# Kernel optimization log

Hardware: AMD Instinct MI355X
Metric: run time of the kernel (lower is better)

## Reference

```python
import jax, jax.numpy as jnp
import numpy as np

B, RES, C = 4, 128, 256
HW = RES * RES
H_FFT, W_FFT = RES, RES // 2 + 1
NUM_BANDS, GATE_HIDDEN = 6, 128
LN_EPS = 1e-5
FFT_NORM = 'ortho'
INIT_RANGE = 0.02


def _band_info(h_fft, w_fft, nb):
    # static radial band partition of the rFFT2 plane (matches RadialBandGate.__init__)
    yy = np.arange(h_fft, dtype=np.float32)[:, None] / max(h_fft - 1, 1)
    xx = np.arange(w_fft, dtype=np.float32)[None, :] / max(w_fft - 1, 1)
    r = np.sqrt(yy ** 2 + xx ** 2)
    r = r / (r.max() + 1e-8)
    bid = np.minimum(np.floor(r * nb), nb - 1).astype(np.int32).reshape(-1)  # (F,)
    onehot = np.zeros((bid.size, nb), dtype=np.float32)
    onehot[np.arange(bid.size), bid] = 1.0
    counts = np.maximum(onehot.sum(0), 1.0)
    return jnp.asarray(bid), jnp.asarray(onehot), jnp.asarray(counts)

BAND_ID, BAND_ONEHOT, BAND_COUNTS = _band_info(H_FFT, W_FFT, NUM_BANDS)


def setup_inputs() -> dict:
    key = jax.random.key(0)
    ks = jax.random.split(key, 16)
    return {
        'x': jax.random.normal(ks[0], (B, HW, C), jnp.float32),
        'time': jax.random.uniform(ks[1], (B,), jnp.float32),
        'w_real': jax.random.normal(ks[2], (C, C), jnp.float32) * INIT_RANGE,
        'w_imag': jax.random.normal(ks[3], (C, C), jnp.float32) * INIT_RANGE,
        'conv_w': jax.random.normal(ks[4], (C, 1, 3, 3), jnp.float32) * 0.1,  # depthwise
        'lin_w': jax.random.normal(ks[5], (C, C), jnp.float32) * 0.02,
        'lin_b': jnp.zeros((C,), jnp.float32),
        'mlp_w1': jax.random.normal(ks[6], (GATE_HIDDEN, NUM_BANDS), jnp.float32) * 0.3,
        'mlp_b1': jnp.zeros((GATE_HIDDEN,), jnp.float32),
        'mlp_w2': jax.random.normal(ks[7], (NUM_BANDS, GATE_HIDDEN), jnp.float32) * 0.1,
        'mlp_b2': jnp.zeros((NUM_BANDS,), jnp.float32),
        'norm_ww': jax.random.normal(ks[8], (C, 1), jnp.float32) * 0.02,  # ConditionalLayerNorm.weight Linear(1,dim)
        'norm_wb': jnp.ones((C,), jnp.float32),
        'norm_bw': jax.random.normal(ks[9], (C, 1), jnp.float32) * 0.02,
        'norm_bb': jnp.zeros((C,), jnp.float32),
        'kx': jnp.asarray(0.25, jnp.float32),
        'ky': jnp.asarray(0.25, jnp.float32),
    }


def _band_gate(feat, mlp_w1, mlp_b1, mlp_w2, mlp_b2):
    # feat: (B, C, F) real. scatter-add per band via one-hot matmul, mean, MLP, gather back.
    sums = jnp.einsum('bcf,fn->bcn', feat, BAND_ONEHOT)           # (B,C,NB)
    means = sums / (BAND_COUNTS + 1e-6)
    h = jax.nn.relu(jnp.einsum('bcn,hn->bch', means, mlp_w1) + mlp_b1)
    alpha_band = jax.nn.sigmoid(jnp.einsum('bch,nh->bcn', h, mlp_w2) + mlp_b2)
    return alpha_band[:, :, BAND_ID]                               # (B,C,F)


def reference(x, time, w_real, w_imag, conv_w, lin_w, lin_b,
              mlp_w1, mlp_b1, mlp_w2, mlp_b2,
              norm_ww, norm_wb, norm_bw, norm_bb, kx, ky):
    h = w = RES
    x2 = jnp.transpose(x.reshape(B, h, w, C), (0, 3, 1, 2))        # (B,C,h,w)
    Xf = jnp.fft.rfft2(x2, norm=FFT_NORM)                          # (B,C,h_fft,w_fft) complex

    # low-frequency rectangular mask (int(sigmoid(k)*dim) == floor for positive values)
    kx_i = jnp.floor(jax.nn.sigmoid(kx) * H_FFT)
    ky_i = jnp.floor(jax.nn.sigmoid(ky) * W_FFT)
    mask = ((jnp.arange(H_FFT)[:, None] < kx_i) & (jnp.arange(W_FFT)[None, :] < ky_i))
    Xf_low = Xf * mask[None, None].astype(Xf.real.dtype)

    F = H_FFT * W_FFT
    Xf_low_flat = Xf_low.reshape(B, C, F)
    W = w_real + 1j * w_imag                                       # (C,C) complex
    Xf_low_mapped = jnp.einsum('cd,bdf->bcf', W, Xf_low_flat).reshape(B, C, H_FFT, W_FFT)

    Xf_high = Xf - Xf_low
    feat_pred = jnp.abs(jnp.abs(Xf_high).reshape(B, C, F) - jnp.abs(Xf_low).reshape(B, C, F))
    alpha = _band_gate(feat_pred, mlp_w1, mlp_b1, mlp_w2, mlp_b2).reshape(B, C, H_FFT, W_FFT)

    Xf_fused = alpha * Xf_low_mapped + (1.0 - alpha) * Xf_high
    x_spec = jnp.fft.irfft2(Xf_fused, s=(h, w), norm=FFT_NORM)     # (B,C,h,w) real

    # depthwise 3x3 conv, padding=1, no bias
    xl = jax.lax.conv_general_dilated(x2, conv_w, window_strides=(1, 1), padding='SAME',
                                      feature_group_count=C,
                                      dimension_numbers=('NCHW', 'OIHW', 'NCHW'))
    # pointwise linear over channel dim
    xc = jnp.transpose((x @ lin_w.T + lin_b).reshape(B, h, w, C), (0, 3, 1, 2))

    y = jnp.transpose(x_spec + xl + xc, (0, 2, 3, 1)).reshape(B, HW, C)

    # ConditionalLayerNorm
    mean = y.mean(axis=-1, keepdims=True)
    var = (y ** 2).mean(axis=-1, keepdims=True) - mean ** 2
    yn = (y - mean) / jnp.sqrt(var + LN_EPS)
    t = time.reshape(-1, 1)                                        # (B,1)
    weight = (t @ norm_ww.T + norm_wb)[:, None, :]                 # (B,1,C)
    bias = (t @ norm_bw.T + norm_bb)[:, None, :]
    return weight * yn + bias
```

## Files before the change

kernel.cpp:

```cpp
#include <hip/hip_runtime.h>
#include <math.h>

#define B_ 4
#define C_ 256
#define RES_ 128
#define HW_ 16384
#define WF_ 65
#define F_ 8320
#define FP_ 2880

typedef __attribute__((ext_vector_type(8))) short bf16x8;
typedef __attribute__((ext_vector_type(16))) float f32x16;

__device__ __forceinline__ int brev6(int j){ return (int)(__brev((unsigned)j) >> 26); }

__device__ __forceinline__ short f2bf(float f){
  unsigned u = __float_as_uint(f);
  unsigned r = (u + 0x7FFFu + ((u>>16)&1u)) >> 16;
  return (short)r;
}

__device__ __forceinline__ bf16x8 lds_frag(const short* p){
  union { bf16x8 v; int2 d[2]; } u;
  u.d[0] = *(const int2*)p;
  u.d[1] = *(const int2*)(p+4);
  return u.v;
}
__device__ __forceinline__ void lds_store8(short* p, bf16x8 v){
  union { bf16x8 v; int2 d[2]; } u; u.v = v;
  *(int2*)p = u.d[0]; *(int2*)(p+4) = u.d[1];
}

__device__ __forceinline__ int band_of(int row, int col){
  float yy = __fdiv_rn((float)row, 127.0f);
  float xx = __fdiv_rn((float)col, 64.0f);
  float rr = __fsqrt_rn(__fadd_rn(__fmul_rn(yy,yy), __fmul_rn(xx,xx)));
  float rm = __fadd_rn(__fsqrt_rn(2.0f), 1e-8f);
  float rn = __fdiv_rn(rr, rm);
  int b = (int)floorf(__fmul_rn(rn, 6.0f));
  return b > 5 ? 5 : b;
}

__device__ __forceinline__ float sigmoidf_(float v){ return 1.0f/(1.0f+expf(-v)); }

template<int SGN>
__device__ __forceinline__ float2 wave_fft64(float2 v, const float2* stw, int lane){
  #pragma unroll
  for (int s=0; s<6; s++){
    int H = 32 >> s;
    float ox = __shfl_xor(v.x, H);
    float oy = __shfl_xor(v.y, H);
    bool hi = (lane & H) != 0;
    float2 w = stw[s];
    float ws = (SGN < 0) ? -w.y : w.y;
    float sx = v.x + ox, sy = v.y + oy;
    float dx = ox - v.x, dy = oy - v.y;
    float rx = dx*w.x - dy*ws;
    float ry = dx*ws + dy*w.x;
    v.x = hi ? rx : sx;
    v.y = hi ? ry : sy;
  }
  return v;
}

__device__ __forceinline__ void make_stage_tw(float2* stw, int lane){
  #pragma unroll
  for (int s=0; s<6; s++){
    int H = 32 >> s;
    int t = (lane & (H-1)) << s;
    float sn, cs;
    sincosf(6.283185307179586f*(float)t/64.0f, &sn, &cs);
    stw[s] = make_float2(cs, sn);
  }
}

__device__ __forceinline__ void redist2(float2 a0, float2 a1, int lane, float2& u0, float2& u1){
  int s0 = lane >> 1, s1 = s0 + 32;
  bool odd = (lane & 1) != 0;
  float t0x = __shfl(a0.x, s0), t0y = __shfl(a0.y, s0);
  float t1x = __shfl(a1.x, s0), t1y = __shfl(a1.y, s0);
  u0 = odd ? make_float2(t1x, t1y) : make_float2(t0x, t0y);
  float q0x = __shfl(a0.x, s1), q0y = __shfl(a0.y, s1);
  float q1x = __shfl(a1.x, s1), q1y = __shfl(a1.y, s1);
  u1 = odd ? make_float2(q1x, q1y) : make_float2(q0x, q0y);
}

__global__ __launch_bounds__(256) void k_transpose(const float* __restrict__ x, float* __restrict__ x2){
  __shared__ float tile[64][68];
  int b = blockIdx.z;
  int hw0 = blockIdx.x*64, c0 = blockIdx.y*64;
  int tid = threadIdx.x;
  #pragma unroll
  for (int q=0;q<4;q++){
    int p = tid + q*256;
    int hw = p >> 4, c4 = (p & 15) << 2;
    float4 v = *(const float4*)&x[((size_t)b*HW_ + hw0 + hw)*C_ + c0 + c4];
    *(float4*)&tile[hw][c4] = v;
  }
  __syncthreads();
  #pragma unroll
  for (int q=0;q<4;q++){
    int p = tid + q*256;
    int c = p >> 4, h4 = (p & 15) << 2;
    float4 v = make_float4(tile[h4][c], tile[h4+1][c], tile[h4+2][c], tile[h4+3][c]);
    *(float4*)&x2[((size_t)b*C_ + c0 + c)*HW_ + hw0 + h4] = v;
  }
}

__global__ __launch_bounds__(256) void k_counts(float* __restrict__ counts, unsigned char* __restrict__ bid_t){
  int tid = threadIdx.x;
  float acc[6] = {0,0,0,0,0,0};
  for (int p = tid; p < F_; p += 256){
    int kx = p >> 7, ky = p & 127;
    int bnd = band_of(ky, kx);
    bid_t[p] = (unsigned char)bnd;
    #pragma unroll
    for (int n=0;n<6;n++) acc[n] += (bnd==n) ? 1.0f : 0.0f;
  }
  __shared__ float red[6][256];
  #pragma unroll
  for (int n=0;n<6;n++) red[n][tid] = acc[n];
  __syncthreads();
  for (int s=128; s>0; s>>=1){
    if (tid < s){
      #pragma unroll
      for (int n=0;n<6;n++) red[n][tid] += red[n][tid+s];
    }
    __syncthreads();
  }
  if (tid < 6) counts[tid] = fmaxf(red[tid][0], 1.0f);
}

__global__ __launch_bounds__(256) void k_wbf16(const float* __restrict__ wre, const float* __restrict__ wim,
                                               const float* __restrict__ lw,
                                               short* __restrict__ Wre, short* __restrict__ Wim,
                                               short* __restrict__ WL){
  int c = blockIdx.x, tid = threadIdx.x, plane = blockIdx.y;
  int idx = c*C_ + tid;
  if (plane == 0)      Wre[idx] = f2bf(wre[idx]);
  else if (plane == 1) Wim[idx] = f2bf(wim[idx]);
  else                 WL[idx]  = f2bf(lw[idx]);
}

__global__ __launch_bounds__(256) void k_fwd_rows(const float* __restrict__ x2, float2* __restrict__ X1t){
  __shared__ float2 tile[65*33];
  int tid = threadIdx.x;
  int lane = tid & 63, wv = tid >> 6;
  float2 stw[6];
  make_stage_tw(stw, lane);
  float sn128, cs128;
  sincosf(6.283185307179586f*(float)lane/128.0f, &sn128, &cs128);
  int slice = blockIdx.x >> 2;
  int r0 = (blockIdx.x & 3) * 32;
  const float* img = x2 + (size_t)slice*HW_ + (size_t)r0*128;
  #pragma unroll
  for (int i=0; i<8; i++){
    int rr = wv*8 + i;
    float2 y = *(const float2*)(img + rr*128 + lane*2);
    float2 v = wave_fft64<-1>(y, stw, lane);
    int rbk = brev6(lane);
    float2 Yk; Yk.x = __shfl(v.x, rbk); Yk.y = __shfl(v.y, rbk);
    int rbm = brev6((64 - lane) & 63);
    float2 Ym; Ym.x = __shfl(v.x, rbm); Ym.y = __shfl(v.y, rbm);
    float sx = Yk.x + Ym.x, sy = Yk.y - Ym.y;
    float dx = Yk.x - Ym.x, dy = Yk.y + Ym.y;
    tile[lane*33 + rr] = make_float2(0.5f*(sx - sn128*dx + cs128*dy),
                                     0.5f*(sy - cs128*dx - sn128*dy));
    if (lane == 0)
      tile[64*33 + rr] = make_float2(Yk.x - Yk.y, 0.0f);
  }
  __syncthreads();
  float2* dst = X1t + (size_t)slice*F_ + r0;
  for (int p = tid; p < 65*16; p += 256){
    int kx = p >> 4, r2 = (p & 15) << 1;
    float2 a = tile[kx*33 + r2], b = tile[kx*33 + r2 + 1];
    *(float4*)(dst + (size_t)kx*128 + r2) = make_float4(a.x, a.y, b.x, b.y);
  }
}

__global__ __launch_bounds__(256) void k_fwd_cols_gate(const float2* __restrict__ X1t, float2* __restrict__ Xft,
                                                       const float* __restrict__ counts, const unsigned char* __restrict__ bid_t,
                                                       const float* __restrict__ w1, const float* __restrict__ b1,
                                                       const float* __restrict__ w2, const float* __restrict__ b2,
                                                       float* __restrict__ alpha){
  __shared__ float red[6][4];
  __shared__ float means[6], h[128];
  int tid = threadIdx.x;
  int lane = tid & 63, wv = tid >> 6;
  float2 stw[6];
  make_stage_tw(stw, lane);
  float sn128, cs128;
  sincosf(6.283185307179586f*(float)lane/128.0f, &sn128, &cs128);
  int slice = blockIdx.x;
  const float2* xin = X1t + (size_t)slice*F_;
  float2* xout = Xft + (size_t)slice*F_;
  float acc[6] = {0,0,0,0,0,0};
  for (int kx = wv; kx < 65; kx += 4){
    float4 rv = *(const float4*)(xin + (size_t)kx*128 + (lane<<1));
    float2 a0 = make_float2(rv.x, rv.y), a1 = make_float2(rv.z, rv.w);
    float2 u0, u1;
    redist2(a0, a1, lane, u0, u1);
    float2 s = make_float2(u0.x+u1.x, u0.y+u1.y);
    float ddx = u0.x-u1.x, ddy = u0.y-u1.y;
    float2 dw = make_float2(ddx*cs128 + ddy*sn128, ddy*cs128 - ddx*sn128);
    float2 v0 = wave_fft64<-1>(s, stw, lane);
    float2 v1 = wave_fft64<-1>(dw, stw, lane);
    int rb = brev6(lane);
    float ex = __shfl(v0.x, rb), ey = __shfl(v0.y, rb);
    float ox = __shfl(v1.x, rb), oy = __shfl(v1.y, rb);
    ex *= 0.0078125f; ey *= 0.0078125f;
    ox *= 0.0078125f; oy *= 0.0078125f;
    float4 wvout = make_float4(ex, ey, ox, oy);
    *(float4*)(xout + (size_t)kx*128 + (lane<<1)) = wvout;
    float me = __fsqrt_rn(ex*ex + ey*ey);
    float mo = __fsqrt_rn(ox*ox + oy*oy);
    int be = (int)bid_t[kx*128 + (lane<<1)];
    int bo = (int)bid_t[kx*128 + (lane<<1) + 1];
    #pragma unroll
    for (int n=0;n<6;n++) acc[n] += ((be==n) ? me : 0.0f) + ((bo==n) ? mo : 0.0f);
  }
  #pragma unroll
  for (int n=0;n<6;n++){
    float v = acc[n];
    #pragma unroll
    for (int off=32; off>0; off>>=1) v += __shfl_xor(v, off);
    if (lane == 0) red[n][wv] = v;
  }
  __syncthreads();
  if (tid < 6) means[tid] = (red[tid][0]+red[tid][1]+red[tid][2]+red[tid][3]) / (counts[tid] + 1e-6f);
  __syncthreads();
  if (tid < 128){
    float hv = b1[tid];
    #pragma unroll
    for (int n=0;n<6;n++) hv += means[n]*w1[tid*6+n];
    h[tid] = fmaxf(hv, 0.0f);
  }
  __syncthreads();
  if (tid < 6){
    float o = b2[tid];
    for (int j=0;j<128;j++) o += h[j]*w2[tid*128+j];
    alpha[slice*6 + tid] = sigmoidf_(o);
  }
}

__global__ __launch_bounds__(256) void k_xt(const float2* __restrict__ Xft,
                                            short* __restrict__ XtRe, short* __restrict__ XtIm){
  __shared__ short sre[72*130];
  __shared__ short sim[72*130];
  int tid = threadIdx.x;
  int kx = blockIdx.x, d0 = blockIdx.y*128, b = blockIdx.z;
  const float2* xb = Xft + ((size_t)(b*C_ + d0))*F_ + (size_t)kx*128;
  for (int p = tid; p < 72*128; p += 256){
    int d = p / 72, ky = p - d*72;
    float2 v = xb[(size_t)d*F_ + ky];
    sre[ky*130 + d] = f2bf(v.x);
    sim[ky*130 + d] = f2bf(v.y);
  }
  __syncthreads();
  short* dre = XtRe + ((size_t)b*FP_ + (size_t)kx*72)*C_ + d0;
  short* dim_ = XtIm + ((size_t)b*FP_ + (size_t)kx*72)*C_ + d0;
  for (int p = tid; p < 72*128; p += 256){
    int ky = p >> 7, d = p & 127;
    dre[(size_t)ky*C_ + d] = sre[ky*130 + d];
    dim_[(size_t)ky*C_ + d] = sim[ky*130 + d];
  }
}

__global__ __launch_bounds__(256) void k_mix_mfma(const short* __restrict__ Wre, const short* __restrict__ Wim,
                                                  const short* __restrict__ XtRe, const short* __restrict__ XtIm,
                                                  const float* __restrict__ kxp, const float* __restrict__ kyp,
                                                  float2* __restrict__ mappedP){
  __shared__ short Are[64][36], Aim[64][36], Bre[64][36], Bim[64][36];
  int tid = threadIdx.x;
  int fp0 = blockIdx.x*64, c0 = blockIdx.y*64, b = blockIdx.z;
  int lane = tid & 63, w = tid >> 6;
  int mt = (w >> 1)*32, nt = (w & 1)*32;
  f32x16 accre = {0.f,0.f,0.f,0.f,0.f,0.f,0.f,0.f,0.f,0.f,0.f,0.f,0.f,0.f,0.f,0.f};
  f32x16 accim = {0.f,0.f,0.f,0.f,0.f,0.f,0.f,0.f,0.f,0.f,0.f,0.f,0.f,0.f,0.f,0.f};
  const short* xrb = XtRe + ((size_t)b*FP_ + fp0)*C_;
  const short* xib = XtIm + ((size_t)b*FP_ + fp0)*C_;
  int row4 = tid >> 2, part = tid & 3;
  for (int kc=0; kc<8; kc++){
    int d0 = kc*32;
    __syncthreads();
    lds_store8(&Are[row4][part*8], *(const bf16x8*)&Wre[(c0+row4)*C_ + d0 + part*8]);
    lds_store8(&Aim[row4][part*8], *(const bf16x8*)&Wim[(c0+row4)*C_ + d0 + part*8]);
    lds_store8(&Bre[row4][part*8], *(const bf16x8*)&xrb[(size_t)row4*C_ + d0 + part*8]);
    lds_store8(&Bim[row4][part*8], *(const bf16x8*)&xib[(size_t)row4*C_ + d0 + part*8]);
    __syncthreads();
    #pragma unroll
    for (int ks=0; ks<2; ks++){
      int koff = ks*16 + (lane>>5)*8;
      bf16x8 are = lds_frag(&Are[mt + (lane&31)][koff]);
      bf16x8 aim = lds_frag(&Aim[mt + (lane&31)][koff]);
      bf16x8 bre = lds_frag(&Bre[nt + (lane&31)][koff]);
      bf16x8 bim = lds_frag(&Bim[nt + (lane&31)][koff]);
      bf16x8 naim;
      { union { bf16x8 v; unsigned u[4]; } t1, t2; t1.v = aim;
        #pragma unroll
        for (int j=0;j<4;j++) t2.u[j] = t1.u[j] ^ 0x80008000u;
        naim = t2.v; }
      accre = __builtin_amdgcn_mfma_f32_32x32x16_bf16(are,  bre, accre, 0,0,0);
      accre = __builtin_amdgcn_mfma_f32_32x32x16_bf16(naim, bim, accre, 0,0,0);
      accim = __builtin_amdgcn_mfma_f32_32x32x16_bf16(are,  bim, accim, 0,0,0);
      accim = __builtin_amdgcn_mfma_f32_32x32x16_bf16(aim,  bre, accim, 0,0,0);
    }
  }
  float rowlim = floorf(sigmoidf_(kxp[0])*128.0f);
  float collim = floorf(sigmoidf_(kyp[0])*65.0f);
  int n = fp0 + nt + (lane & 31);
  int ky = n % 72, kx = n / 72;
  bool live = ((float)ky < rowlim) && ((float)kx < collim);
  #pragma unroll
  for (int reg=0; reg<16; reg++){
    int r = (reg & 3) + 8*(reg >> 2) + 4*(lane >> 5);
    int c = c0 + mt + r;
    if (live)
      mappedP[((size_t)(b*C_ + c))*FP_ + n] = make_float2(accre[reg], accim[reg]);
  }
}

__global__ __launch_bounds__(256) void k_pw_mfma(const float* __restrict__ x, const short* __restrict__ WL,
                                                  const float* __restrict__ lb, float* __restrict__ xcs){
  __shared__ short As[64][36], Bs[64][36];
  int tid = threadIdx.x;
  int hw0 = blockIdx.x*64, c0 = blockIdx.y*64, b = blockIdx.z;
  int lane = tid & 63, w = tid >> 6;
  int mt = (w >> 1)*32, nt = (w & 1)*32;
  f32x16 acc = {0.f,0.f,0.f,0.f,0.f,0.f,0.f,0.f,0.f,0.f,0.f,0.f,0.f,0.f,0.f,0.f};
  const float* xb = x + ((size_t)b*HW_ + hw0)*C_;
  int row4 = tid >> 2, part = tid & 3;
  for (int kc=0; kc<8; kc++){
    int d0 = kc*32;
    __syncthreads();
    lds_store8(&As[row4][part*8], *(const bf16x8*)&WL[(c0+row4)*C_ + d0 + part*8]);
    {
      const float* src = &xb[(size_t)row4*C_ + d0 + part*8];
      float4 va = *(const float4*)src;
      float4 vb = *(const float4*)(src+4);
      bf16x8 bv;
      bv[0]=f2bf(va.x); bv[1]=f2bf(va.y); bv[2]=f2bf(va.z); bv[3]=f2bf(va.w);
      bv[4]=f2bf(vb.x); bv[5]=f2bf(vb.y); bv[6]=f2bf(vb.z); bv[7]=f2bf(vb.w);
      lds_store8(&Bs[row4][part*8], bv);
    }
    __syncthreads();
    #pragma unroll
    for (int ks=0; ks<2; ks++){
      int koff = ks*16 + (lane>>5)*8;
      bf16x8 a  = lds_frag(&As[mt + (lane&31)][koff]);
      bf16x8 bb = lds_frag(&Bs[nt + (lane&31)][koff]);
      acc = __builtin_amdgcn_mfma_f32_32x32x16_bf16(a, bb, acc, 0,0,0);
    }
  }
  int n = hw0 + nt + (lane & 31);
  #pragma unroll
  for (int reg=0; reg<16; reg++){
    int r = (reg & 3) + 8*(reg >> 2) + 4*(lane >> 5);
    int c = c0 + mt + r;
    xcs[((size_t)(b*C_ + c))*HW_ + n] = acc[reg] + lb[c];
  }
}

__global__ __launch_bounds__(256) void k_inv_cols(float2* __restrict__ XftY, const float2* __restrict__ mappedP,
                                                  const float* __restrict__ alpha, const unsigned char* __restrict__ bid_t,
                                                  const float* __restrict__ kxp, const float* __restrict__ kyp){
  __shared__ float al[6];
  int tid = threadIdx.x;
  int lane = tid & 63, wv = tid >> 6;
  int slice = blockIdx.x;
  float2 stw[6];
  make_stage_tw(stw, lane);
  float sn128, cs128;
  sincosf(6.283185307179586f*(float)lane/128.0f, &sn128, &cs128);
  if (tid < 6) al[tid] = alpha[slice*6 + tid];
  float rowlim = floorf(sigmoidf_(kxp[0])*128.0f);
  float collim = floorf(sigmoidf_(kyp[0])*65.0f);
  __syncthreads();
  float2* xfb = XftY + (size_t)slice*F_;
  const float2* mpb = mappedP + (size_t)slice*FP_;
  for (int kx = wv; kx < 65; kx += 4){
    float4 rv = *(const float4*)(xfb + (size_t)kx*128 + (lane<<1));
    int ky0 = lane << 1;
    float a_e = al[(int)bid_t[kx*128 + ky0]];
    float a_o = al[(int)bid_t[kx*128 + ky0 + 1]];
    bool cok  = ((float)kx < collim);
    bool in_e = cok && ((float)ky0 < rowlim);
    bool in_o = cok && ((float)(ky0+1) < rowlim);
    float2 ve, vo;
    if (in_e){
      float4 mv = *(const float4*)(mpb + (size_t)kx*72 + ky0);
      ve = make_float2(mv.x*a_e, mv.y*a_e);
      vo = in_o ? make_float2(mv.z*a_o, mv.w*a_o)
                : make_float2(rv.z*(1.0f-a_o), rv.w*(1.0f-a_o));
    } else {
      ve = make_float2(rv.x*(1.0f-a_e), rv.y*(1.0f-a_e));
      vo = make_float2(rv.z*(1.0f-a_o), rv.w*(1.0f-a_o));
    }
    float2 u0, u1;
    redist2(ve, vo, lane, u0, u1);
    float2 s = make_float2(u0.x+u1.x, u0.y+u1.y);
    float ddx = u0.x-u1.x, ddy = u0.y-u1.y;
    float2 dw = make_float2(ddx*cs128 - ddy*sn128, ddx*sn128 + ddy*cs128);
    float2 v0 = wave_fft64<1>(s, stw, lane);
    float2 v1 = wave_fft64<1>(dw, stw, lane);
    int rb = brev6(lane);
    float4 outv;
    outv.x = __shfl(v0.x, rb); outv.y = __shfl(v0.y, rb);
    outv.z = __shfl(v1.x, rb); outv.w = __shfl(v1.y, rb);
    *(float4*)(xfb + (size_t)kx*128 + (lane<<1)) = outv;
  }
}

__global__ __launch_bounds__(256,8) void k_inv_rows(const float2* __restrict__ Y1t, const float* __restrict__ xcs,
                                                    const float* __restrict__ x2, const float* __restrict__ cw,
                                                    float* __restrict__ sbuf){
  __shared__ float2 ytile[65*33];
  int tid = threadIdx.x;
  int lane = tid & 63, wv = tid >> 6;
  float2 stw[6];
  make_stage_tw(stw, lane);
  float sn128, cs128;
  sincosf(6.283185307179586f*(float)lane/128.0f, &sn128, &cs128);
  int slice = blockIdx.x >> 2;
  int ch = slice & 255;
  int r0 = (blockIdx.x & 3) * 32;
  const float* img = x2 + (size_t)slice*HW_;
  int base = r0 + wv*8;
  float2 rows[10];
  #pragma unroll
  for (int i=0;i<10;i++){
    int gr = base - 1 + i;
    rows[i] = ((unsigned)gr < 128u) ? *(const float2*)(img + (size_t)gr*128 + (lane<<1))
                                    : make_float2(0.0f, 0.0f);
  }
  const float2* ysrc = Y1t + (size_t)slice*F_ + r0;
  for (int p = tid; p < 65*16; p += 256){
    int kx = p >> 4, r2 = (p & 15) << 1;
    float4 v = *(const float4*)(ysrc + (size_t)kx*128 + r2);
    ytile[kx*33 + r2]     = make_float2(v.x, v.y);
    ytile[kx*33 + r2 + 1] = make_float2(v.z, v.w);
  }
  float w9[9];
  #pragma unroll
  for (int k=0;k<9;k++) w9[k] = cw[ch*9+k];
  __syncthreads();
  size_t gbase = (size_t)slice*HW_ + (size_t)r0*128;
  #pragma unroll
  for (int i=0;i<8;i++){
    int row = wv*8 + i;
    float2 a = ytile[lane*33 + row];
    float2 b = ytile[(64-lane)*33 + row];
    if (lane == 0){ a.y = 0.0f; b.y = 0.0f; }
    float sx = a.x + b.x, sy = a.y - b.y;
    float dx = a.x - b.x, dy = a.y + b.y;
    float2 yk = make_float2(0.5f*(sx - sn128*dx - cs128*dy),
                            0.5f*(sy + cs128*dx - sn128*dy));
    float2 v = wave_fft64<1>(yk, stw, lane);
    int rbk = brev6(lane);
    float2 z; z.x = __shfl(v.x, rbk); z.y = __shfl(v.y, rbk);
    int xx = lane << 1;
    float c0 = 0.0f, c1 = 0.0f;
    #pragma unroll
    for (int dy2=0; dy2<3; dy2++){
      float2 cv = rows[i + dy2];
      float l = __shfl_up(cv.y, 1);
      if (lane == 0) l = 0.0f;
      float r = __shfl_down(cv.x, 1);
      if (lane == 63) r = 0.0f;
      c0 += l*w9[dy2*3+0] + cv.x*w9[dy2*3+1] + cv.y*w9[dy2*3+2];
      c1 += cv.x*w9[dy2*3+0] + cv.y*w9[dy2*3+1] + r*w9[dy2*3+2];
    }
    size_t g = gbase + (size_t)(row*128 + xx);
    float2 xc = *(const float2*)&xcs[g];
    float2 o;
    o.x = z.x*0.015625f + xc.x + c0;
    o.y = z.y*0.015625f + xc.y + c1;
    *(float2*)&sbuf[g] = o;
  }
}

__global__ __launch_bounds__(256) void k_norm(const float* __restrict__ sbuf, const float* __restrict__ timev,
                                              const float* __restrict__ nww, const float* __restrict__ nwb,
                                              const float* __restrict__ nbw, const float* __restrict__ nbb,
                                              float* __restrict__ out){
  __shared__ float tile[64][65];
  __shared__ float p1[64][5], p2[64][5];
  __shared__ float mv[64], rv[64], wv_[256], bv_[256];
  int b = blockIdx.y, hw0 = blockIdx.x*64;
  int tid = threadIdx.x;
  {
    float t = timev[b];
    wv_[tid] = t*nww[tid] + nwb[tid];
    bv_[tid] = t*nbw[tid] + nbb[tid];
  }
  int hwl = tid & 63, cg = tid >> 6;
  const float* p = sbuf + (size_t)b*C_*HW_ + hw0 + hwl;
  float s1 = 0.0f, s2 = 0.0f;
  for (int c = cg*64; c < cg*64 + 64; c++){
    float v = p[(size_t)c*HW_];
    s1 += v; s2 += v*v;
  }
  p1[hwl][cg] = s1; p2[hwl][cg] = s2;
  __syncthreads();
  if (tid < 64){
    float t1 = p1[tid][0] + p1[tid][1] + p1[tid][2] + p1[tid][3];
    float t2 = p2[tid][0] + p2[tid][1] + p2[tid][2] + p2[tid][3];
    float mean = t1 * (1.0f/256.0f);
    float var  = t2 * (1.0f/256.0f) - mean*mean;
    mv[tid] = mean;
    rv[tid] = 1.0f / sqrtf(var + 1e-5f);
  }
  __syncthreads();
  for (int cg2=0; cg2<4; cg2++){
    int c0 = cg2*64;
    #pragma unroll
    for (int q=0;q<16;q++){
      int pp = tid + q*256;
      int cl = pp >> 6, hl = pp & 63;
      tile[cl][hl] = sbuf[((size_t)(b*C_ + c0 + cl))*HW_ + hw0 + hl];
    }
    __syncthreads();
    #pragma unroll
    for (int q=0;q<16;q++){
      int pp = tid + q*256;
      int hl = pp >> 6, cl = pp & 63;
      float v = tile[cl][hl];
      out[((size_t)(b*HW_ + hw0 + hl))*C_ + c0 + cl] = wv_[c0+cl]*((v - mv[hl])*rv[hl]) + bv_[c0+cl];
    }
    __syncthreads();
  }
}

extern "C" void kernel_launch(void* const* d_in, const int* in_sizes, int n_in,
                              void* d_out, int out_size, void* d_ws, size_t ws_size,
                              hipStream_t stream){
  const float* x      = (const float*)d_in[0];
  const float* timev  = (const float*)d_in[1];
  const float* w_real = (const float*)d_in[2];
  const float* w_imag = (const float*)d_in[3];
  const float* conv_w = (const float*)d_in[4];
  const float* lin_w  = (const float*)d_in[5];
  const float* lin_b  = (const float*)d_in[6];
  const float* mlp_w1 = (const float*)d_in[7];
  const float* mlp_b1 = (const float*)d_in[8];
  const float* mlp_w2 = (const float*)d_in[9];
  const float* mlp_b2 = (const float*)d_in[10];
  const float* norm_ww= (const float*)d_in[11];
  const float* norm_wb= (const float*)d_in[12];
  const float* norm_bw= (const float*)d_in[13];
  const float* norm_bb= (const float*)d_in[14];
  const float* kxp    = (const float*)d_in[15];
  const float* kyp    = (const float*)d_in[16];

  float* ws = (float*)d_ws;
  float*  alpha  = ws;
  unsigned char* bid_t = (unsigned char*)(ws + 6144);
  float*  counts = ws + 8224;
  short*  Wre_bf = (short*)(ws + 139360);
  short*  Wim_bf = (short*)(ws + 172128);
  short*  WL_bf  = (short*)(ws + 204896);
  float*  x2     = ws + 237664;
  float2* Xft    = (float2*)(ws + 17014880);
  float*  CbF    = ws + 34054240;
  float2* X1t    = (float2*)CbF;
  short*  XtRe   = (short*)CbF;
  short*  XtIm   = (short*)(CbF + 1474560);
  float2* mappedP= (float2*)(CbF + 2949120);
  float*  sb     = CbF;
  float*  xcs    = (float*)d_out;
  float*  out    = (float*)d_out;

  k_transpose    <<<dim3(256, 4, B_), 256, 0, stream>>>(x, x2);
  k_counts       <<<1, 256, 0, stream>>>(counts, bid_t);
  k_wbf16        <<<dim3(256, 3), 256, 0, stream>>>(w_real, w_imag, lin_w, Wre_bf, Wim_bf, WL_bf);
  k_fwd_rows     <<<4096, 256, 0, stream>>>(x2, X1t);
  k_fwd_cols_gate<<<1024, 256, 0, stream>>>(X1t, Xft, counts, bid_t, mlp_w1, mlp_b1, mlp_w2, mlp_b2, alpha);
  k_xt           <<<dim3(40, 2, B_), 256, 0, stream>>>(Xft, XtRe, XtIm);
  k_pw_mfma      <<<dim3(256, 4, B_), 256, 0, stream>>>(x, WL_bf, lin_b, xcs);
  k_mix_mfma     <<<dim3(45, 4, B_), 256, 0, stream>>>(Wre_bf, Wim_bf, XtRe, XtIm, kxp, kyp, mappedP);
  k_inv_cols     <<<1024, 256, 0, stream>>>(Xft, mappedP, alpha, bid_t, kxp, kyp);
  k_inv_rows     <<<4096, 256, 0, stream>>>((const float2*)Xft, xcs, x2, conv_w, sb);
  k_norm         <<<dim3(256, B_), 256, 0, stream>>>(sb, timev, norm_ww, norm_wb, norm_bw, norm_bb, out);
}
```

Measured before the change: 438.8 us.

## Fuse row and column FFT passes into single per-slice kernels via LDS

Merges the forward row-FFT and column-FFT/gate kernels into one 512-thread kernel per (batch, channel) slice that keeps the whole 65x128 intermediate spectrum in LDS. The inverse column and row passes plus the conv and residual are fused the same way. This removes the X1t global round trip and the Y1t write-back and reread between passes. In exchange it uses about 67 KB of LDS per block and 18 preloaded rows per thread, which lowers occupancy and the number of blocks from 4096 to 1024. The sb buffer moves to a separate offset because Xft is no longer overwritten in place.

```diff
diff --git a/kernel.cpp b/kernel.cpp
--- a/kernel.cpp
+++ b/kernel.cpp
@@ -142,20 +142,25 @@
   else                 WL[idx]  = f2bf(lw[idx]);
 }
 
-__global__ __launch_bounds__(256) void k_fwd_rows(const float* __restrict__ x2, float2* __restrict__ X1t){
-  __shared__ float2 tile[65*33];
+__global__ __launch_bounds__(512) void k_fwd(const float* __restrict__ x2, float2* __restrict__ Xft,
+                                             const float* __restrict__ counts, const unsigned char* __restrict__ bid_t,
+                                             const float* __restrict__ w1, const float* __restrict__ b1,
+                                             const float* __restrict__ w2, const float* __restrict__ b2,
+                                             float* __restrict__ alpha){
+  __shared__ float2 lt[65*129];
+  __shared__ float red[6][8];
+  __shared__ float means[6], h[128];
   int tid = threadIdx.x;
   int lane = tid & 63, wv = tid >> 6;
   float2 stw[6];
   make_stage_tw(stw, lane);
   float sn128, cs128;
   sincosf(6.283185307179586f*(float)lane/128.0f, &sn128, &cs128);
-  int slice = blockIdx.x >> 2;
-  int r0 = (blockIdx.x & 3) * 32;
-  const float* img = x2 + (size_t)slice*HW_ + (size_t)r0*128;
-  #pragma unroll
-  for (int i=0; i<8; i++){
-    int rr = wv*8 + i;
+  int slice = blockIdx.x;
+  const float* img = x2 + (size_t)slice*HW_;
+  #pragma unroll
+  for (int i=0; i<16; i++){
+    int rr = wv*16 + i;
     float2 y = *(const float2*)(img + rr*128 + lane*2);
     float2 v = wave_fft64<-1>(y, stw, lane);
     int rbk = brev6(lane);
@@ -164,40 +169,17 @@
     float2 Ym; Ym.x = __shfl(v.x, rbm); Ym.y = __shfl(v.y, rbm);
     float sx = Yk.x + Ym.x, sy = Yk.y - Ym.y;
     float dx = Yk.x - Ym.x, dy = Yk.y + Ym.y;
-    tile[lane*33 + rr] = make_float2(0.5f*(sx - sn128*dx + cs128*dy),
-                                     0.5f*(sy - cs128*dx - sn128*dy));
+    lt[lane*129 + rr] = make_float2(0.5f*(sx - sn128*dx + cs128*dy),
+                                    0.5f*(sy - cs128*dx - sn128*dy));
     if (lane == 0)
-      tile[64*33 + rr] = make_float2(Yk.x - Yk.y, 0.0f);
-  }
-  __syncthreads();
-  float2* dst = X1t + (size_t)slice*F_ + r0;
-  for (int p = tid; p < 65*16; p += 256){
-    int kx = p >> 4, r2 = (p & 15) << 1;
-    float2 a = tile[kx*33 + r2], b = tile[kx*33 + r2 + 1];
-    *(float4*)(dst + (size_t)kx*128 + r2) = make_float4(a.x, a.y, b.x, b.y);
-  }
-}
-
-__global__ __launch_bounds__(256) void k_fwd_cols_gate(const float2* __restrict__ X1t, float2* __restrict__ Xft,
-                                                       const float* __restrict__ counts, const unsigned char* __restrict__ bid_t,
-                                                       const float* __restrict__ w1, const float* __restrict__ b1,
-                                                       const float* __restrict__ w2, const float* __restrict__ b2,
-                                                       float* __restrict__ alpha){
-  __shared__ float red[6][4];
-  __shared__ float means[6], h[128];
-  int tid = threadIdx.x;
-  int lane = tid & 63, wv = tid >> 6;
-  float2 stw[6];
-  make_stage_tw(stw, lane);
-  float sn128, cs128;
-  sincosf(6.283185307179586f*(float)lane/128.0f, &sn128, &cs128);
-  int slice = blockIdx.x;
-  const float2* xin = X1t + (size_t)slice*F_;
+      lt[64*129 + rr] = make_float2(Yk.x - Yk.y, 0.0f);
+  }
+  __syncthreads();
   float2* xout = Xft + (size_t)slice*F_;
   float acc[6] = {0,0,0,0,0,0};
-  for (int kx = wv; kx < 65; kx += 4){
-    float4 rv = *(const float4*)(xin + (size_t)kx*128 + (lane<<1));
-    float2 a0 = make_float2(rv.x, rv.y), a1 = make_float2(rv.z, rv.w);
+  for (int kx = wv; kx < 65; kx += 8){
+    float2 a0 = lt[kx*129 + (lane<<1)];
+    float2 a1 = lt[kx*129 + (lane<<1) + 1];
     float2 u0, u1;
     redist2(a0, a1, lane, u0, u1);
     float2 s = make_float2(u0.x+u1.x, u0.y+u1.y);
@@ -210,8 +192,7 @@
     float ox = __shfl(v1.x, rb), oy = __shfl(v1.y, rb);
     ex *= 0.0078125f; ey *= 0.0078125f;
     ox *= 0.0078125f; oy *= 0.0078125f;
-    float4 wvout = make_float4(ex, ey, ox, oy);
-    *(float4*)(xout + (size_t)kx*128 + (lane<<1)) = wvout;
+    *(float4*)(xout + (size_t)kx*128 + (lane<<1)) = make_float4(ex, ey, ox, oy);
     float me = __fsqrt_rn(ex*ex + ey*ey);
     float mo = __fsqrt_rn(ox*ox + oy*oy);
     int be = (int)bid_t[kx*128 + (lane<<1)];
@@ -227,7 +208,12 @@
     if (lane == 0) red[n][wv] = v;
   }
   __syncthreads();
-  if (tid < 6) means[tid] = (red[tid][0]+red[tid][1]+red[tid][2]+red[tid][3]) / (counts[tid] + 1e-6f);
+  if (tid < 6){
+    float t = 0.0f;
+    #pragma unroll
+    for (int q=0;q<8;q++) t += red[tid][q];
+    means[tid] = t / (counts[tid] + 1e-6f);
+  }
   __syncthreads();
   if (tid < 128){
     float hv = b1[tid];
@@ -361,24 +347,40 @@
   }
 }
 
-__global__ __launch_bounds__(256) void k_inv_cols(float2* __restrict__ XftY, const float2* __restrict__ mappedP,
-                                                  const float* __restrict__ alpha, const unsigned char* __restrict__ bid_t,
-                                                  const float* __restrict__ kxp, const float* __restrict__ kyp){
+__global__ __launch_bounds__(512) void k_inv(const float2* __restrict__ Xft, const float2* __restrict__ mappedP,
+                                             const float* __restrict__ alpha, const unsigned char* __restrict__ bid_t,
+                                             const float* __restrict__ kxp, const float* __restrict__ kyp,
+                                             const float* __restrict__ xcs, const float* __restrict__ x2,
+                                             const float* __restrict__ cw, float* __restrict__ sbuf){
+  __shared__ float2 lt[65*129];
   __shared__ float al[6];
   int tid = threadIdx.x;
   int lane = tid & 63, wv = tid >> 6;
-  int slice = blockIdx.x;
   float2 stw[6];
   make_stage_tw(stw, lane);
   float sn128, cs128;
   sincosf(6.283185307179586f*(float)lane/128.0f, &sn128, &cs128);
+  int slice = blockIdx.x;
+  int ch = slice & 255;
   if (tid < 6) al[tid] = alpha[slice*6 + tid];
   float rowlim = floorf(sigmoidf_(kxp[0])*128.0f);
   float collim = floorf(sigmoidf_(kyp[0])*65.0f);
-  __syncthreads();
-  float2* xfb = XftY + (size_t)slice*F_;
+  const float* img = x2 + (size_t)slice*HW_;
+  int base = wv*16;
+  float2 rows[18];
+  #pragma unroll
+  for (int i=0;i<18;i++){
+    int gr = base - 1 + i;
+    rows[i] = ((unsigned)gr < 128u) ? *(const float2*)(img + (size_t)gr*128 + (lane<<1))
+                                    : make_float2(0.0f, 0.0f);
+  }
+  float w9[9];
+  #pragma unroll
+  for (int k=0;k<9;k++) w9[k] = cw[ch*9+k];
+  __syncthreads();
+  const float2* xfb = Xft + (size_t)slice*F_;
   const float2* mpb = mappedP + (size_t)slice*FP_;
-  for (int kx = wv; kx < 65; kx += 4){
+  for (int kx = wv; kx < 65; kx += 8){
     float4 rv = *(const float4*)(xfb + (size_t)kx*128 + (lane<<1));
     int ky0 = lane << 1;
     float a_e = al[(int)bid_t[kx*128 + ky0]];
@@ -404,52 +406,18 @@
     float2 v0 = wave_fft64<1>(s, stw, lane);
     float2 v1 = wave_fft64<1>(dw, stw, lane);
     int rb = brev6(lane);
-    float4 outv;
-    outv.x = __shfl(v0.x, rb); outv.y = __shfl(v0.y, rb);
-    outv.z = __shfl(v1.x, rb); outv.w = __shfl(v1.y, rb);
-    *(float4*)(xfb + (size_t)kx*128 + (lane<<1)) = outv;
-  }
-}
-
-__global__ __launch_bounds__(256,8) void k_inv_rows(const float2* __restrict__ Y1t, const float* __restrict__ xcs,
-                                                    const float* __restrict__ x2, const float* __restrict__ cw,
-                                                    float* __restrict__ sbuf){
-  __shared__ float2 ytile[65*33];
-  int tid = threadIdx.x;
-  int lane = tid & 63, wv = tid >> 6;
-  float2 stw[6];
-  make_stage_tw(stw, lane);
-  float sn128, cs128;
-  sincosf(6.283185307179586f*(float)lane/128.0f, &sn128, &cs128);
-  int slice = blockIdx.x >> 2;
-  int ch = slice & 255;
-  int r0 = (blockIdx.x & 3) * 32;
-  const float* img = x2 + (size_t)slice*HW_;
-  int base = r0 + wv*8;
-  float2 rows[10];
-  #pragma unroll
-  for (int i=0;i<10;i++){
-    int gr = base - 1 + i;
-    rows[i] = ((unsigned)gr < 128u) ? *(const float2*)(img + (size_t)gr*128 + (lane<<1))
-                                    : make_float2(0.0f, 0.0f);
-  }
-  const float2* ysrc = Y1t + (size_t)slice*F_ + r0;
-  for (int p = tid; p < 65*16; p += 256){
-    int kx = p >> 4, r2 = (p & 15) << 1;
-    float4 v = *(const float4*)(ysrc + (size_t)kx*128 + r2);
-    ytile[kx*33 + r2]     = make_float2(v.x, v.y);
-    ytile[kx*33 + r2 + 1] = make_float2(v.z, v.w);
-  }
-  float w9[9];
-  #pragma unroll
-  for (int k=0;k<9;k++) w9[k] = cw[ch*9+k];
-  __syncthreads();
-  size_t gbase = (size_t)slice*HW_ + (size_t)r0*128;
-  #pragma unroll
-  for (int i=0;i<8;i++){
-    int row = wv*8 + i;
-    float2 a = ytile[lane*33 + row];
-    float2 b = ytile[(64-lane)*33 + row];
+    float2 z0; z0.x = __shfl(v0.x, rb); z0.y = __shfl(v0.y, rb);
+    float2 z1; z1.x = __shfl(v1.x, rb); z1.y = __shfl(v1.y, rb);
+    lt[kx*129 + ky0]     = z0;
+    lt[kx*129 + ky0 + 1] = z1;
+  }
+  __syncthreads();
+  size_t gbase = (size_t)slice*HW_;
+  #pragma unroll
+  for (int i=0;i<16;i++){
+    int row = base + i;
+    float2 a = lt[lane*129 + row];
+    float2 b = lt[(64-lane)*129 + row];
     if (lane == 0){ a.y = 0.0f; b.y = 0.0f; }
     float sx = a.x + b.x, sy = a.y - b.y;
     float dx = a.x - b.x, dy = a.y + b.y;
@@ -562,23 +530,20 @@
   float*  x2     = ws + 237664;
   float2* Xft    = (float2*)(ws + 17014880);
   float*  CbF    = ws + 34054240;
-  float2* X1t    = (float2*)CbF;
   short*  XtRe   = (short*)CbF;
   short*  XtIm   = (short*)(CbF + 1474560);
   float2* mappedP= (float2*)(CbF + 2949120);
-  float*  sb     = CbF;
+  float*  sb     = CbF + 8847360;
   float*  xcs    = (float*)d_out;
   float*  out    = (float*)d_out;
 
   k_transpose    <<<dim3(256, 4, B_), 256, 0, stream>>>(x, x2);
   k_counts       <<<1, 256, 0, stream>>>(counts, bid_t);
   k_wbf16        <<<dim3(256, 3), 256, 0, stream>>>(w_real, w_imag, lin_w, Wre_bf, Wim_bf, WL_bf);
-  k_fwd_rows     <<<4096, 256, 0, stream>>>(x2, X1t);
-  k_fwd_cols_gate<<<1024, 256, 0, stream>>>(X1t, Xft, counts, bid_t, mlp_w1, mlp_b1, mlp_w2, mlp_b2, alpha);
+  k_fwd          <<<1024, 512, 0, stream>>>(x2, Xft, counts, bid_t, mlp_w1, mlp_b1, mlp_w2, mlp_b2, alpha);
   k_xt           <<<dim3(40, 2, B_), 256, 0, stream>>>(Xft, XtRe, XtIm);
   k_pw_mfma      <<<dim3(256, 4, B_), 256, 0, stream>>>(x, WL_bf, lin_b, xcs);
   k_mix_mfma     <<<dim3(45, 4, B_), 256, 0, stream>>>(Wre_bf, Wim_bf, XtRe, XtIm, kxp, kyp, mappedP);
-  k_inv_cols     <<<1024, 256, 0, stream>>>(Xft, mappedP, alpha, bid_t, kxp, kyp);
-  k_inv_rows     <<<4096, 256, 0, stream>>>((const float2*)Xft, xcs, x2, conv_w, sb);
+  k_inv          <<<1024, 512, 0, stream>>>(Xft, mappedP, alpha, bid_t, kxp, kyp, xcs, x2, conv_w, sb);
   k_norm         <<<dim3(256, B_), 256, 0, stream>>>(sb, timev, norm_ww, norm_wb, norm_bw, norm_bb, out);
 }
```

New measurement: 424.1 us. 3.3% less time.
